# Optimization experiments

Hardware: AMD Instinct MI355X
Metric: run time of the kernel (lower is better)

The kernel has to match this reference:

```python
import jax, jax.numpy as jnp
import numpy as np

B = 16
SR = 16000
DUR = 3
L = SR * DUR          # 48000 samples
W = 64                # n_wavetables
LWT = 512             # wavetable_len


def setup_inputs() -> dict:
    key = jax.random.key(0)
    k1, k2, k3, k4 = jax.random.split(key, 4)
    # Per-sample F0 in a realistic range (CREPE-style, upsampled to sr)
    pitch = jax.random.uniform(k1, (B, L), dtype=jnp.float32, minval=50.0, maxval=500.0)
    envelope = jax.random.uniform(k2, (B, L, 1), dtype=jnp.float32)
    # attention is "already softmaxed" per the docstring
    attention = jax.nn.softmax(jax.random.normal(k3, (B, L, W), dtype=jnp.float32), axis=-1)
    # Wavetable bank: first 4 are fixed sines with cycles 1..4, rest N(0, 0.01)
    i = jnp.arange(LWT, dtype=jnp.float32)
    fixed = jnp.stack([jnp.sin(c * 2.0 * jnp.pi * i / LWT) for c in (1, 2, 3, 4)], axis=0)
    learned = 0.01 * jax.random.normal(k4, (W - 4, LWT), dtype=jnp.float32)
    wavetables = jnp.concatenate([fixed, learned], axis=0)  # [W, LWT]
    return {"pitch": pitch, "envelope": envelope, "attention": attention, "wavetables": wavetables}


def reference(pitch, envelope, attention, wavetables):
    lwt = wavetables.shape[1]
    # phase increment per sample, per batch item: [B, L]
    increment = (lwt / SR) * pitch
    # NOTE: faithful to original torch code: subtracts the FIRST BATCH ROW
    # of increments (broadcast over batch), not a per-row first element.
    index = jnp.cumsum(increment, axis=1) - increment[0]
    index = jnp.remainder(index, lwt)
    index = jnp.where(lwt - index < 1e-05, 0.0, index)
    low = jnp.floor(index)
    alpha = index - low                       # [B, L]
    idx_low = low.astype(jnp.int32)           # in [0, lwt-1]
    idx_high = jnp.ceil(index).astype(jnp.int32) % lwt
    # Dual gather across all 64 wavetables at once: [W, B, L]
    wl = wavetables[:, idx_low]
    wh = wavetables[:, idx_high]
    waves = wl + alpha[None, :, :] * (wh - wl)  # linear interpolation
    # attention-weighted sum over wavetables, then envelope: [B, L, 1]
    out = jnp.einsum('wbl,blw->bl', waves, attention)[..., None] * envelope
    return out
```

## Files before the change

### kernel.cpp

```cpp
#include <hip/hip_runtime.h>
#include <hip/hip_fp16.h>

#define BB    16
#define LL    48000
#define WW    64
#define LWT   512
#define CHUNK 750
#define NCH   64
#define NELEM (BB*LL)
#define NGRP  (NELEM/4)
#define RATIO (512.0/16000.0)

__global__ void kT(const float* __restrict__ wt, __half* __restrict__ tab) {
    int tid = blockIdx.x * 256 + threadIdx.x;
    int idx = tid >> 6, w = tid & 63;
    tab[tid] = __float2half(wt[w * LWT + idx]);
}

__global__ void kA(const float* __restrict__ pitch, double* __restrict__ csum) {
    int bid = blockIdx.x;
    int r = bid >> 6, c = bid & 63;
    int t = threadIdx.x;
    double s = 0.0;
    if (t < 250) {
        const float* p = pitch + r * LL + c * CHUNK + t * 3;
        s = RATIO * (double)p[0] + RATIO * (double)p[1] + RATIO * (double)p[2];
    }
    for (int d = 1; d < 64; d <<= 1) s += __shfl_xor(s, d);
    __shared__ double wsh[4];
    if ((t & 63) == 0) wsh[t >> 6] = s;
    __syncthreads();
    if (t == 0) csum[bid] = wsh[0] + wsh[1] + wsh[2] + wsh[3];
}

__global__ void kB(const double* __restrict__ csum, double* __restrict__ cbase) {
    int r = threadIdx.x >> 6, c = threadIdx.x & 63;
    double v = csum[r * NCH + c];
    double inc = v;
    for (int d = 1; d < 64; d <<= 1) {
        double u = __shfl_up(inc, d);
        if (c >= d) inc += u;
    }
    cbase[r * NCH + c] = inc - v;
}

__global__ void kC(const float* __restrict__ pitch,
                   const double* __restrict__ cbase,
                   unsigned* __restrict__ packed) {
    int bid = blockIdx.x;
    int r = bid >> 6, c = bid & 63;
    int t = threadIdx.x;
    int lane = t & 63, wv = t >> 6;
    int l = c * CHUNK + t * 3;
    bool act = (t < 250);
    double i0 = 0.0, i1 = 0.0, i2 = 0.0;
    if (act) {
        const float* p = pitch + r * LL + l;
        i0 = RATIO * (double)p[0];
        i1 = RATIO * (double)p[1];
        i2 = RATIO * (double)p[2];
    }
    double c0 = i0, c1 = i0 + i1, c2 = c1 + i2;
    double inc = c2;
    for (int d = 1; d < 64; d <<= 1) {
        double u = __shfl_up(inc, d);
        if (lane >= d) inc += u;
    }
    __shared__ double wsum[4];
    if (lane == 63) wsum[wv] = inc;
    __syncthreads();
    double wb = 0.0;
    for (int i = 0; i < wv; i++) wb += wsum[i];
    if (!act) return;
    double base = cbase[bid] + (wb + inc - c2);
    double pre[3] = {c0, c1, c2};
    for (int k = 0; k < 3; k++) {
        double inc0 = RATIO * (double)pitch[l + k];
        double idx = base + pre[k] - inc0;
        double m = idx - floor(idx * (1.0 / 512.0)) * 512.0;
        if (m < 0.0) m += 512.0;
        if (512.0 - m < 1e-5) m = 0.0;
        double lowd = floor(m);
        double alpha = m - lowd;
        unsigned il = (unsigned)lowd;
        unsigned au = (unsigned)(alpha * 8388608.0 + 0.5);
        if (au > 0x7fffffu) au = 0x7fffffu;
        packed[r * LL + l + k] = (il << 23) | au;
    }
}

__global__ __launch_bounds__(256) void kD(const float4* __restrict__ attn4,
                                          const float* __restrict__ env,
                                          const unsigned* __restrict__ packed,
                                          const __half* __restrict__ tabG,
                                          float* __restrict__ out) {
    __shared__ __half tab[LWT * WW];
    {
        const uint4* s4 = (const uint4*)tabG;
        uint4* d4 = (uint4*)tab;
        for (int i = threadIdx.x; i < (LWT * WW) / 8; i += 256) d4[i] = s4[i];
    }
    __syncthreads();
    const int lane = threadIdx.x & 63;
    const int sub = lane >> 4;
    const int li  = lane & 15;
    const int wid = (blockIdx.x << 2) | (threadIdx.x >> 6);
    const int gpw = 94;
    int g0 = wid * gpw;
    int g1 = g0 + gpw;
    if (g1 > NGRP) g1 = NGRP;
    if (g0 >= g1) return;

    float4  a = attn4[(size_t)g0 * 64 + lane];
    unsigned p = packed[(g0 << 2) | sub];
    for (int g = g0; g < g1; ++g) {
        float4 ac = a;
        unsigned pc = p;
        int gn = g + 1;
        if (gn < g1) {
            a = attn4[(size_t)gn * 64 + lane];
            p = packed[(gn << 2) | sub];
        }
        unsigned il = pc >> 23;
        float alpha = (float)(pc & 0x7fffffu) * (1.0f / 8388608.0f);
        unsigned ih = (il + 1) & 511;
        uint2 lo = *(const uint2*)(tab + (il << 6) + (li << 2));
        uint2 hi = *(const uint2*)(tab + (ih << 6) + (li << 2));
        __half2 l01 = *(__half2*)&lo.x, l23 = *(__half2*)&lo.y;
        __half2 h01 = *(__half2*)&hi.x, h23 = *(__half2*)&hi.y;
        float2 fl01 = __half22float2(l01), fl23 = __half22float2(l23);
        float2 fh01 = __half22float2(h01), fh23 = __half22float2(h23);
        float w0 = fmaf(alpha, fh01.x - fl01.x, fl01.x);
        float w1 = fmaf(alpha, fh01.y - fl01.y, fl01.y);
        float w2 = fmaf(alpha, fh23.x - fl23.x, fl23.x);
        float w3 = fmaf(alpha, fh23.y - fl23.y, fl23.y);
        float s = w0 * ac.x + w1 * ac.y + w2 * ac.z + w3 * ac.w;
        s += __shfl_xor(s, 1);
        s += __shfl_xor(s, 2);
        s += __shfl_xor(s, 4);
        s += __shfl_xor(s, 8);
        if (li == 0) {
            int e = (g << 2) | sub;
            out[e] = s * env[e];
        }
    }
}

extern "C" void kernel_launch(void* const* d_in, const int* in_sizes, int n_in,
                              void* d_out, int out_size, void* d_ws, size_t ws_size,
                              hipStream_t stream) {
    const float* pitch = (const float*)d_in[0];
    const float* env   = (const float*)d_in[1];
    const float* attn  = (const float*)d_in[2];
    const float* wt    = (const float*)d_in[3];
    float* out = (float*)d_out;

    char* ws = (char*)d_ws;
    __half*   tab    = (__half*)(ws);
    double*   csum   = (double*)(ws + 65536);
    double*   cbase  = (double*)(ws + 73728);
    unsigned* packed = (unsigned*)(ws + 81920);

    kT<<<128, 256, 0, stream>>>(wt, tab);
    kA<<<BB * NCH, 256, 0, stream>>>(pitch, csum);
    kB<<<1, 1024, 0, stream>>>(csum, cbase);
    kC<<<BB * NCH, 256, 0, stream>>>(pitch, cbase, packed);
    kD<<<512, 256, 0, stream>>>((const float4*)attn, env, packed, tab, out);
}
```

Baseline: 321.2 us.

## Fuse prefix-scan kernels and table transpose, use grid-stride kD

Replaces the three-kernel chunked prefix sum (kA/kB/kC) with a single kP kernel that uses one 1024-thread block per batch row, where each thread serially scans 48 elements. The separate wavetable transpose kernel is folded into kD, with each block converting fp32 to fp16 into LDS. kD moves to 1024-thread blocks with grid-stride interleaved groups instead of contiguous per-wave ranges. The aim is to cut launch count and intermediate buffers, at the cost of a very low-parallelism scan (16 blocks, strided serial loads) and redundant per-block table conversion from global memory.

Result: no change. 324.4 us (+1.0%).

```diff
diff --git a/kernel.cpp b/kernel.cpp
--- a/kernel.cpp
+++ b/kernel.cpp
@@ -5,119 +5,84 @@
 #define LL    48000
 #define WW    64
 #define LWT   512
-#define CHUNK 750
-#define NCH   64
 #define NELEM (BB*LL)
 #define NGRP  (NELEM/4)
 #define RATIO (512.0/16000.0)
+#define EPT   48
+#define KD_BLOCKS 512
+#define KD_WAVES  (KD_BLOCKS*16)
 
-__global__ void kT(const float* __restrict__ wt, __half* __restrict__ tab) {
-    int tid = blockIdx.x * 256 + threadIdx.x;
-    int idx = tid >> 6, w = tid & 63;
-    tab[tid] = __float2half(wt[w * LWT + idx]);
-}
+__global__ __launch_bounds__(1024) void kP(const float* __restrict__ pitch,
+                                           unsigned* __restrict__ packed) {
+    const int r = blockIdx.x;
+    const int t = threadIdx.x;
+    const bool act = (t < 1000);
+    const int e0 = t * EPT;
+    const float* prow = pitch + (size_t)r * LL;
 
-__global__ void kA(const float* __restrict__ pitch, double* __restrict__ csum) {
-    int bid = blockIdx.x;
-    int r = bid >> 6, c = bid & 63;
-    int t = threadIdx.x;
     double s = 0.0;
-    if (t < 250) {
-        const float* p = pitch + r * LL + c * CHUNK + t * 3;
-        s = RATIO * (double)p[0] + RATIO * (double)p[1] + RATIO * (double)p[2];
+    if (act) {
+        for (int k = 0; k < EPT; k++) s += RATIO * (double)prow[e0 + k];
     }
-    for (int d = 1; d < 64; d <<= 1) s += __shfl_xor(s, d);
-    __shared__ double wsh[4];
-    if ((t & 63) == 0) wsh[t >> 6] = s;
-    __syncthreads();
-    if (t == 0) csum[bid] = wsh[0] + wsh[1] + wsh[2] + wsh[3];
-}
-
-__global__ void kB(const double* __restrict__ csum, double* __restrict__ cbase) {
-    int r = threadIdx.x >> 6, c = threadIdx.x & 63;
-    double v = csum[r * NCH + c];
-    double inc = v;
-    for (int d = 1; d < 64; d <<= 1) {
-        double u = __shfl_up(inc, d);
-        if (c >= d) inc += u;
-    }
-    cbase[r * NCH + c] = inc - v;
-}
-
-__global__ void kC(const float* __restrict__ pitch,
-                   const double* __restrict__ cbase,
-                   unsigned* __restrict__ packed) {
-    int bid = blockIdx.x;
-    int r = bid >> 6, c = bid & 63;
-    int t = threadIdx.x;
-    int lane = t & 63, wv = t >> 6;
-    int l = c * CHUNK + t * 3;
-    bool act = (t < 250);
-    double i0 = 0.0, i1 = 0.0, i2 = 0.0;
-    if (act) {
-        const float* p = pitch + r * LL + l;
-        i0 = RATIO * (double)p[0];
-        i1 = RATIO * (double)p[1];
-        i2 = RATIO * (double)p[2];
-    }
-    double c0 = i0, c1 = i0 + i1, c2 = c1 + i2;
-    double inc = c2;
+    const int lane = t & 63, wv = t >> 6;
+    double inc = s;
     for (int d = 1; d < 64; d <<= 1) {
         double u = __shfl_up(inc, d);
         if (lane >= d) inc += u;
     }
-    __shared__ double wsum[4];
+    __shared__ double wsum[16];
     if (lane == 63) wsum[wv] = inc;
     __syncthreads();
     double wb = 0.0;
     for (int i = 0; i < wv; i++) wb += wsum[i];
     if (!act) return;
-    double base = cbase[bid] + (wb + inc - c2);
-    double pre[3] = {c0, c1, c2};
-    for (int k = 0; k < 3; k++) {
-        double inc0 = RATIO * (double)pitch[l + k];
-        double idx = base + pre[k] - inc0;
+    double run = wb + inc - s;
+
+    const float* p0 = pitch;
+    unsigned* prow_out = packed + (size_t)r * LL;
+    for (int k = 0; k < EPT; k++) {
+        int l = e0 + k;
+        run += RATIO * (double)prow[l];
+        double idx = run - RATIO * (double)p0[l];
         double m = idx - floor(idx * (1.0 / 512.0)) * 512.0;
-        if (m < 0.0) m += 512.0;
+        if (m < 0.0)    m += 512.0;
+        if (m >= 512.0) m -= 512.0;
         if (512.0 - m < 1e-5) m = 0.0;
         double lowd = floor(m);
         double alpha = m - lowd;
         unsigned il = (unsigned)lowd;
         unsigned au = (unsigned)(alpha * 8388608.0 + 0.5);
         if (au > 0x7fffffu) au = 0x7fffffu;
-        packed[r * LL + l + k] = (il << 23) | au;
+        prow_out[l] = (il << 23) | au;
     }
 }
 
-__global__ __launch_bounds__(256) void kD(const float4* __restrict__ attn4,
-                                          const float* __restrict__ env,
-                                          const unsigned* __restrict__ packed,
-                                          const __half* __restrict__ tabG,
-                                          float* __restrict__ out) {
+__global__ __launch_bounds__(1024, 8) void kD(const float4* __restrict__ attn4,
+                                              const float* __restrict__ env,
+                                              const unsigned* __restrict__ packed,
+                                              const float* __restrict__ wt,
+                                              float* __restrict__ out) {
     __shared__ __half tab[LWT * WW];
-    {
-        const uint4* s4 = (const uint4*)tabG;
-        uint4* d4 = (uint4*)tab;
-        for (int i = threadIdx.x; i < (LWT * WW) / 8; i += 256) d4[i] = s4[i];
+    for (int i = threadIdx.x; i < LWT * WW; i += 1024) {
+        int w = i >> 9, idx = i & 511;
+        tab[(idx << 6) | w] = __float2half(wt[i]);
     }
     __syncthreads();
+
     const int lane = threadIdx.x & 63;
     const int sub = lane >> 4;
     const int li  = lane & 15;
-    const int wid = (blockIdx.x << 2) | (threadIdx.x >> 6);
-    const int gpw = 94;
-    int g0 = wid * gpw;
-    int g1 = g0 + gpw;
-    if (g1 > NGRP) g1 = NGRP;
-    if (g0 >= g1) return;
+    const int wid = (blockIdx.x << 4) | (threadIdx.x >> 6);
 
-    float4  a = attn4[(size_t)g0 * 64 + lane];
-    unsigned p = packed[(g0 << 2) | sub];
-    for (int g = g0; g < g1; ++g) {
+    int g = wid;
+    if (g >= NGRP) return;
+    float4  a = attn4[(size_t)g * 64 + lane];
+    unsigned p = packed[(g << 2) | sub];
+    while (true) {
         float4 ac = a;
         unsigned pc = p;
-        int gn = g + 1;
-        if (gn < g1) {
+        int gn = g + KD_WAVES;
+        if (gn < NGRP) {
             a = attn4[(size_t)gn * 64 + lane];
             p = packed[(gn << 2) | sub];
         }
@@ -134,15 +99,17 @@
         float w1 = fmaf(alpha, fh01.y - fl01.y, fl01.y);
         float w2 = fmaf(alpha, fh23.x - fl23.x, fl23.x);
         float w3 = fmaf(alpha, fh23.y - fl23.y, fl23.y);
-        float s = w0 * ac.x + w1 * ac.y + w2 * ac.z + w3 * ac.w;
-        s += __shfl_xor(s, 1);
-        s += __shfl_xor(s, 2);
-        s += __shfl_xor(s, 4);
-        s += __shfl_xor(s, 8);
+        float sv = w0 * ac.x + w1 * ac.y + w2 * ac.z + w3 * ac.w;
+        sv += __shfl_xor(sv, 1);
+        sv += __shfl_xor(sv, 2);
+        sv += __shfl_xor(sv, 4);
+        sv += __shfl_xor(sv, 8);
         if (li == 0) {
             int e = (g << 2) | sub;
-            out[e] = s * env[e];
+            out[e] = sv * env[e];
         }
+        if (gn >= NGRP) break;
+        g = gn;
     }
 }
 
@@ -155,15 +122,8 @@
     const float* wt    = (const float*)d_in[3];
     float* out = (float*)d_out;
 
-    char* ws = (char*)d_ws;
-    __half*   tab    = (__half*)(ws);
-    double*   csum   = (double*)(ws + 65536);
-    double*   cbase  = (double*)(ws + 73728);
-    unsigned* packed = (unsigned*)(ws + 81920);
+    unsigned* packed = (unsigned*)d_ws;
 
-    kT<<<128, 256, 0, stream>>>(wt, tab);
-    kA<<<BB * NCH, 256, 0, stream>>>(pitch, csum);
-    kB<<<1, 1024, 0, stream>>>(csum, cbase);
-    kC<<<BB * NCH, 256, 0, stream>>>(pitch, cbase, packed);
-    kD<<<512, 256, 0, stream>>>((const float4*)attn, env, packed, tab, out);
+    kP<<<BB, 1024, 0, stream>>>(pitch, packed);
+    kD<<<KD_BLOCKS, 1024, 0, stream>>>((const float4*)attn, env, packed, wt, out);
 }
```
